# Kernel optimization log

Hardware: AMD Instinct MI355X
Metric: run time of the kernel (lower is better)

Reference implementation:

```python
import jax, jax.numpy as jnp
import numpy as np

N_HEADS, N_LEVELS, N_POINTS, D_MODEL = 8, 4, 4, 256
HEAD_DIM = D_MODEL // N_HEADS
SPATIAL = np.array([[128, 128], [64, 64], [32, 32], [16, 16]], dtype=np.int32)
LEN_IN = int((SPATIAL[:, 0] * SPATIAL[:, 1]).sum())  # 21760
B = 2


def setup_inputs() -> dict:
    key = jax.random.key(0)
    ks = jax.random.split(key, 8)
    level_start = np.concatenate([[0], np.cumsum(SPATIAL[:, 0] * SPATIAL[:, 1])[:-1]]).astype(np.int32)
    return {
        "query": jax.random.normal(ks[0], (B, LEN_IN, D_MODEL), jnp.float32),
        "reference_points": jax.random.uniform(ks[1], (B, LEN_IN, 2), jnp.float32),
        "input_flatten": jax.random.normal(ks[2], (B, LEN_IN, D_MODEL), jnp.float32),
        "spatial_shapes": jnp.asarray(SPATIAL),
        "level_start_index": jnp.asarray(level_start),
        "W_off": jax.random.normal(ks[3], (D_MODEL, N_HEADS * N_LEVELS * N_POINTS * 2), jnp.float32) * 0.02,
        "b_off": jnp.zeros((N_HEADS * N_LEVELS * N_POINTS * 2,), jnp.float32),
        "W_attn": jax.random.normal(ks[4], (D_MODEL, N_HEADS * N_LEVELS * N_POINTS), jnp.float32) * 0.02,
        "b_attn": jnp.zeros((N_HEADS * N_LEVELS * N_POINTS,), jnp.float32),
        "W_out": jax.random.normal(ks[5], (D_MODEL, D_MODEL), jnp.float32) * 0.02,
        "b_out": jnp.zeros((D_MODEL,), jnp.float32),
    }


def _ms_deform_attn(query, reference_points, input_flatten, spatial_np,
                    W_off, b_off, W_attn, b_attn, W_out, b_out):
    Bq, Lq, C = query.shape
    # sampling offsets / attention weights projections (GEMMs)
    off = (query @ W_off + b_off).reshape(Bq, Lq, N_HEADS, N_LEVELS, N_POINTS, 2)
    attn = (query @ W_attn + b_attn).reshape(Bq, Lq, N_HEADS, N_LEVELS * N_POINTS)
    attn = jax.nn.softmax(attn, axis=-1).reshape(Bq, Lq, N_HEADS, N_LEVELS, N_POINTS)
    # offset normalizer is (W, H) per level
    norm = jnp.asarray(spatial_np[:, ::-1].copy(), jnp.float32)  # [L,2]
    # normalized sampling locations (x,y) in [0,1]: [B,Lq,h,L,p,2]
    loc = reference_points[:, :, None, None, None, :] + off / norm[None, None, None, :, None, :]

    b_idx = jnp.arange(Bq)[:, None, None, None]
    h_idx = jnp.arange(N_HEADS)[None, None, :, None]
    out = jnp.zeros((Bq, Lq, N_HEADS, HEAD_DIM), query.dtype)
    start = 0
    for lvl in range(N_LEVELS):
        H, W = int(spatial_np[lvl, 0]), int(spatial_np[lvl, 1])
        feat = input_flatten[:, start:start + H * W].reshape(Bq, H, W, N_HEADS, HEAD_DIM)
        start += H * W
        # grid_sample(align_corners=False): pixel = loc * size - 0.5
        x = loc[:, :, :, lvl, :, 0] * W - 0.5  # [B,Lq,h,p]
        y = loc[:, :, :, lvl, :, 1] * H - 0.5
        x0 = jnp.floor(x); y0 = jnp.floor(y)
        fx = x - x0; fy = y - y0
        x0i = x0.astype(jnp.int32); y0i = y0.astype(jnp.int32)

        def gather(ix, iy):
            valid = (ix >= 0) & (ix < W) & (iy >= 0) & (iy < H)  # zero padding
            ixc = jnp.clip(ix, 0, W - 1); iyc = jnp.clip(iy, 0, H - 1)
            v = feat[b_idx, iyc, ixc, h_idx]  # [B,Lq,h,p,hd]
            return v * valid[..., None].astype(v.dtype)

        v00 = gather(x0i, y0i)
        v01 = gather(x0i + 1, y0i)
        v10 = gather(x0i, y0i + 1)
        v11 = gather(x0i + 1, y0i + 1)
        sampled = (v00 * ((1 - fx) * (1 - fy))[..., None]
                   + v01 * (fx * (1 - fy))[..., None]
                   + v10 * ((1 - fx) * fy)[..., None]
                   + v11 * (fx * fy)[..., None])  # [B,Lq,h,p,hd]
        out = out + (sampled * attn[:, :, :, lvl, :, None]).sum(axis=3)
    return out.reshape(Bq, Lq, C) @ W_out + b_out


def reference(query, reference_points, input_flatten, spatial_shapes, level_start_index,
              W_off, b_off, W_attn, b_attn, W_out, b_out):
    spatial_np = np.asarray(jax.device_get(spatial_shapes))
    return _ms_deform_attn(query, reference_points, input_flatten, spatial_np,
                           W_off, b_off, W_attn, b_attn, W_out, b_out)
```

## Files before the change

### kernel.cpp

```cpp
#include <hip/hip_runtime.h>
#include <hip/hip_fp16.h>
#include <math.h>

#define BATCH   2
#define LQ      21760
#define CDIM    256
#define NHEADS  8
#define NLEV    4
#define NPTS    4
#define HDIM    32
#define NPROJ   384
#define QT      16
#define PROJ_LD 388
#define NTUP    (QT * NHEADS * NLEV * NPTS)

typedef short  bf16x8 __attribute__((ext_vector_type(8)));
typedef float  f32x4  __attribute__((ext_vector_type(4)));

static __device__ __host__ inline unsigned short f2bf(float x) {
    unsigned int u = __builtin_bit_cast(unsigned int, x);
    unsigned int r = (u + 0x7fff + ((u >> 16) & 1)) >> 16;
    return (unsigned short)r;
}
static __device__ inline unsigned int pack2h(float a, float b) {
    __half2 h = __floats2half2_rn(a, b);
    return __builtin_bit_cast(unsigned int, h);
}
static __device__ inline float2 unpack2h(unsigned int u) {
    return __half22float2(__builtin_bit_cast(__half2, u));
}

__global__ __launch_bounds__(256) void pack_w(
    const float* __restrict__ Woff, const float* __restrict__ Wattn,
    const float* __restrict__ Wout, unsigned short* __restrict__ ws)
{
    const int id = blockIdx.x * 256 + threadIdx.x;
    bf16x8 pk;
    if (id < 12288) {
        const int lane = id & 63, s = (id >> 6) & 7, tn = id >> 9;
        const int col = tn * 16 + (lane & 15);
        const int k0  = s * 32 + (lane >> 4) * 8;
        #pragma unroll
        for (int i = 0; i < 8; ++i) {
            const int k = k0 + i;
            const float w = (col < 256) ? Woff[(size_t)k * 256 + col]
                                        : Wattn[(size_t)k * 128 + (col - 256)];
            pk[i] = (short)f2bf(w);
        }
        *(bf16x8*)(ws + (size_t)id * 8) = pk;
    } else {
        const int id2 = id - 12288;
        const int lane = id2 & 63, s = (id2 >> 6) & 7, tn = id2 >> 9;
        const int col = tn * 16 + (lane & 15);
        const int k0  = s * 32 + (lane >> 4) * 8;
        #pragma unroll
        for (int i = 0; i < 8; ++i)
            pk[i] = (short)f2bf(Wout[(size_t)(k0 + i) * 256 + col]);
        *(bf16x8*)(ws + (size_t)(12288 + id2) * 8) = pk;
    }
}

static __device__ inline void load_afrags(const unsigned char* xqb, int lane, bf16x8* af) {
    const int row = lane & 15;
    const int kg8 = (lane >> 4) * 8;
    const int sw  = (row & 7) << 4;
    const int base = row * 512;
    #pragma unroll
    for (int s = 0; s < 8; ++s) {
        const int byte = base + (((s * 32 + kg8) * 2) ^ sw);
        af[s] = *(const bf16x8*)(xqb + byte);
    }
}

__global__ __launch_bounds__(256, 4) void msda_fused(
    const float* __restrict__ query,
    const float* __restrict__ refp,
    const float* __restrict__ feat,
    const float* __restrict__ boff,
    const float* __restrict__ battn,
    const float* __restrict__ bout,
    const unsigned short* __restrict__ wsB,
    const unsigned short* __restrict__ wsO,
    float* __restrict__ out)
{
    __shared__ __align__(16) unsigned char xqb[QT * 512];
    __shared__ __align__(16) float proj[QT * PROJ_LD];
    __shared__ float rp[QT][2];

    const int t    = threadIdx.x;
    const int lane = t & 63;
    const int wid  = t >> 6;
    const int q0   = blockIdx.x * QT;
    const int b    = q0 / LQ;

    #define PROJ(q, c) proj[(q) * PROJ_LD + (c)]
    int*          toff = (int*)proj;
    unsigned int* tw01 = (unsigned int*)proj + NTUP;
    unsigned int* tw23 = (unsigned int*)proj + 2 * NTUP;

    {
        const float4* src = (const float4*)(query + (size_t)q0 * CDIM);
        #pragma unroll
        for (int i = 0; i < 4; ++i) {
            const int idx = t + i * 256;
            const int row = idx >> 6;
            const int k4  = (idx & 63) * 4;
            const float4 v = src[idx];
            uint2 w;
            w.x = (unsigned int)f2bf(v.x) | ((unsigned int)f2bf(v.y) << 16);
            w.y = (unsigned int)f2bf(v.z) | ((unsigned int)f2bf(v.w) << 16);
            const int byte = row * 512 + (((k4 * 2)) ^ ((row & 7) << 4));
            *(uint2*)(xqb + byte) = w;
        }
        if (t < QT * 2) ((float*)rp)[t] = refp[(size_t)q0 * 2 + t];
    }
    __syncthreads();

    {
        bf16x8 af[8];
        load_afrags(xqb, lane, af);
        const int colb = lane & 15;
        const int r0   = (lane >> 4) * 4;
        #pragma unroll
        for (int j = 0; j < 6; ++j) {
            const int tn  = wid * 6 + j;
            const int col = tn * 16 + colb;
            const float bv = (col < 256) ? boff[col] : battn[col - 256];
            f32x4 acc = {bv, bv, bv, bv};
            const bf16x8* bp = (const bf16x8*)wsB + (size_t)tn * 8 * 64 + lane;
            #pragma unroll
            for (int s = 0; s < 8; ++s)
                acc = __builtin_amdgcn_mfma_f32_16x16x32_bf16(af[s], bp[(size_t)s * 64], acc, 0, 0, 0);
            #pragma unroll
            for (int r = 0; r < 4; ++r) PROJ(r0 + r, col) = acc[r];
        }
    }
    __syncthreads();

    if (t < QT * NHEADS) {
        const int q = t >> 3, h = t & 7;
        float* a = &PROJ(q, CDIM + h * 16);
        float m = a[0];
        #pragma unroll
        for (int j = 1; j < 16; ++j) m = fmaxf(m, a[j]);
        float e[16], s = 0.f;
        #pragma unroll
        for (int j = 0; j < 16; ++j) { e[j] = __expf(a[j] - m); s += e[j]; }
        const float inv = 1.f / s;
        #pragma unroll
        for (int j = 0; j < 16; ++j) a[j] = e[j] * inv;
    }
    __syncthreads();

    int   r_off[8];
    unsigned int r_w01[8], r_w23[8];
    {
        const int LW[4] = {128, 64, 32, 16};
        const int LS[4] = {0, 16384, 20480, 21504};
        #pragma unroll
        for (int k = 0; k < 8; ++k) {
            const int tupid = t * 8 + k;
            const int q  = tupid >> 7;
            const int h  = (tupid >> 4) & 7;
            const int lp = tupid & 15;
            const int l  = lp >> 2, p = lp & 3;
            const int Wl = LW[l], Hl = LW[l];
            const float ox = PROJ(q, ((h * NLEV + l) * NPTS + p) * 2 + 0);
            const float oy = PROJ(q, ((h * NLEV + l) * NPTS + p) * 2 + 1);
            const float aw = PROJ(q, CDIM + h * 16 + lp);
            const float x = rp[q][0] * (float)Wl + ox - 0.5f;
            const float y = rp[q][1] * (float)Hl + oy - 0.5f;
            const float x0f = floorf(x), y0f = floorf(y);
            const float fx = x - x0f, fy = y - y0f;
            const int ix = (int)x0f, iy = (int)y0f;
            const bool vx0 = (ix >= 0) & (ix < Wl), vx1 = (ix >= -1) & (ix < Wl - 1);
            const bool vy0 = (iy >= 0) & (iy < Hl), vy1 = (iy >= -1) & (iy < Hl - 1);
            const float w00 = (vx0 & vy0) ? (1.f - fx) * (1.f - fy) * aw : 0.f;
            const float w01 = (vx1 & vy0) ? fx * (1.f - fy) * aw : 0.f;
            const float w10 = (vx0 & vy1) ? (1.f - fx) * fy * aw : 0.f;
            const float w11 = (vx1 & vy1) ? fx * fy * aw : 0.f;
            r_off[k] = LS[l] + iy * Wl + ix;
            r_w01[k] = pack2h(w00, w01);
            r_w23[k] = pack2h(w10, w11);
        }
    }
    __syncthreads();
    #pragma unroll
    for (int k = 0; k < 8; ++k) {
        const int tupid = t * 8 + k;
        toff[tupid] = r_off[k];
        tw01[tupid] = r_w01[k];
        tw23[tupid] = r_w23[k];
    }
    __syncthreads();

    {
        const int qg = t >> 6, h = (t >> 3) & 7, d4 = t & 7;
        const float* featb = feat + (size_t)b * LQ * CDIM + h * HDIM + d4 * 4;
        #pragma unroll
        for (int j = 0; j < 4; ++j) {
            const int q = qg * 4 + j;
            const int tbase = (q * 8 + h) * 16;
            f32x4 acc = {0.f, 0.f, 0.f, 0.f};
            #pragma unroll
            for (int lp = 0; lp < 16; ++lp) {
                const int Wl = (lp < 4) ? 128 : (lp < 8) ? 64 : (lp < 12) ? 32 : 16;
                const int off00 = toff[tbase + lp];
                const float2 wlo = unpack2h(tw01[tbase + lp]);
                const float2 whi = unpack2h(tw23[tbase + lp]);
                const int o0 = (wlo.x != 0.f) ? off00          : 0;
                const int o1 = (wlo.y != 0.f) ? off00 + 1      : 0;
                const int o2 = (whi.x != 0.f) ? off00 + Wl     : 0;
                const int o3 = (whi.y != 0.f) ? off00 + Wl + 1 : 0;
                const f32x4 v0 = *(const f32x4*)(featb + (long)o0 * CDIM);
                const f32x4 v1 = *(const f32x4*)(featb + (long)o1 * CDIM);
                const f32x4 v2 = *(const f32x4*)(featb + (long)o2 * CDIM);
                const f32x4 v3 = *(const f32x4*)(featb + (long)o3 * CDIM);
                acc += wlo.x * v0;
                acc += wlo.y * v1;
                acc += whi.x * v2;
                acc += whi.y * v3;
            }
            uint2 wv;
            wv.x = (unsigned int)f2bf(acc[0]) | ((unsigned int)f2bf(acc[1]) << 16);
            wv.y = (unsigned int)f2bf(acc[2]) | ((unsigned int)f2bf(acc[3]) << 16);
            const int byte = q * 512 + (((h * HDIM + d4 * 4) * 2) ^ ((q & 7) << 4));
            *(uint2*)(xqb + byte) = wv;
        }
    }
    __syncthreads();

    {
        bf16x8 af[8];
        load_afrags(xqb, lane, af);
        const int colb = lane & 15;
        const int r0   = (lane >> 4) * 4;
        #pragma unroll
        for (int j = 0; j < 4; ++j) {
            const int tn  = wid * 4 + j;
            const int col = tn * 16 + colb;
            const float bv = bout[col];
            f32x4 acc = {bv, bv, bv, bv};
            const bf16x8* bp = (const bf16x8*)wsO + (size_t)tn * 8 * 64 + lane;
            #pragma unroll
            for (int s = 0; s < 8; ++s)
                acc = __builtin_amdgcn_mfma_f32_16x16x32_bf16(af[s], bp[(size_t)s * 64], acc, 0, 0, 0);
            #pragma unroll
            for (int r = 0; r < 4; ++r)
                out[(size_t)(q0 + r0 + r) * CDIM + col] = acc[r];
        }
    }
    #undef PROJ
}

extern "C" void kernel_launch(void* const* d_in, const int* in_sizes, int n_in,
                              void* d_out, int out_size, void* d_ws, size_t ws_size,
                              hipStream_t stream) {
    const float* query = (const float*)d_in[0];
    const float* refp  = (const float*)d_in[1];
    const float* feat  = (const float*)d_in[2];
    const float* Woff  = (const float*)d_in[5];
    const float* boff  = (const float*)d_in[6];
    const float* Wattn = (const float*)d_in[7];
    const float* battn = (const float*)d_in[8];
    const float* Wout  = (const float*)d_in[9];
    const float* bout  = (const float*)d_in[10];
    float* out = (float*)d_out;

    unsigned short* ws = (unsigned short*)d_ws;
    const unsigned short* wsB = ws;
    const unsigned short* wsO = ws + (size_t)12288 * 8;

    hipLaunchKernelGGL(pack_w, dim3(80), dim3(256), 0, stream, Woff, Wattn, Wout, ws);

    const int nrows = BATCH * LQ;
    hipLaunchKernelGGL(msda_fused, dim3(nrows / QT), dim3(256), 0, stream,
                       query, refp, feat, boff, battn, bout, wsB, wsO, out);
}
```

Baseline: 159.1 us.

## Pre-pack features to bf16, shuffle sampling tuples via registers, fp16 projection LDS

Adds a pre-pass that converts the value tensor to bf16 in workspace, so the bilinear gather reads half the bytes per sample. Sampling offsets and weights are passed between lanes with wave shuffles instead of being staged in shared memory. The projection buffer is stored as fp16, which shrinks LDS use enough to raise the occupancy hint to 5 blocks per CU. In exchange, every call pays a full extra read and write of the feature tensor, and offsets and weights lose precision; an fp32 fallback path remains for when the workspace is too small.

```diff
diff --git a/kernel.cpp b/kernel.cpp
--- a/kernel.cpp
+++ b/kernel.cpp
@@ -9,13 +9,13 @@
 #define NLEV    4
 #define NPTS    4
 #define HDIM    32
-#define NPROJ   384
 #define QT      16
-#define PROJ_LD 388
-#define NTUP    (QT * NHEADS * NLEV * NPTS)
+#define PROJ_LDH 392
 
 typedef short  bf16x8 __attribute__((ext_vector_type(8)));
 typedef float  f32x4  __attribute__((ext_vector_type(4)));
+typedef unsigned int u32x4 __attribute__((ext_vector_type(4)));
+typedef unsigned short u16x8 __attribute__((ext_vector_type(8)));
 
 static __device__ __host__ inline unsigned short f2bf(float x) {
     unsigned int u = __builtin_bit_cast(unsigned int, x);
@@ -29,10 +29,29 @@
 static __device__ inline float2 unpack2h(unsigned int u) {
     return __half22float2(__builtin_bit_cast(__half2, u));
 }
+static __device__ inline float bfhi(unsigned int u) {
+    return __builtin_bit_cast(float, u & 0xffff0000u);
+}
+static __device__ inline float bflo(unsigned int u) {
+    return __builtin_bit_cast(float, u << 16);
+}
+
+__global__ __launch_bounds__(256) void pack_feat(
+    const float* __restrict__ f, unsigned short* __restrict__ o)
+{
+    const size_t i8 = ((size_t)blockIdx.x * 256 + threadIdx.x) * 8;
+    const float4 v0 = *(const float4*)(f + i8);
+    const float4 v1 = *(const float4*)(f + i8 + 4);
+    u16x8 pk;
+    pk[0] = f2bf(v0.x); pk[1] = f2bf(v0.y); pk[2] = f2bf(v0.z); pk[3] = f2bf(v0.w);
+    pk[4] = f2bf(v1.x); pk[5] = f2bf(v1.y); pk[6] = f2bf(v1.z); pk[7] = f2bf(v1.w);
+    *(u16x8*)(o + i8) = pk;
+}
 
 __global__ __launch_bounds__(256) void pack_w(
     const float* __restrict__ Woff, const float* __restrict__ Wattn,
-    const float* __restrict__ Wout, unsigned short* __restrict__ ws)
+    const float* __restrict__ Wout, unsigned short* __restrict__ wsB,
+    unsigned short* __restrict__ wsO)
 {
     const int id = blockIdx.x * 256 + threadIdx.x;
     bf16x8 pk;
@@ -47,7 +66,7 @@
                                         : Wattn[(size_t)k * 128 + (col - 256)];
             pk[i] = (short)f2bf(w);
         }
-        *(bf16x8*)(ws + (size_t)id * 8) = pk;
+        *(bf16x8*)(wsB + (size_t)id * 8) = pk;
     } else {
         const int id2 = id - 12288;
         const int lane = id2 & 63, s = (id2 >> 6) & 7, tn = id2 >> 9;
@@ -56,7 +75,7 @@
         #pragma unroll
         for (int i = 0; i < 8; ++i)
             pk[i] = (short)f2bf(Wout[(size_t)(k0 + i) * 256 + col]);
-        *(bf16x8*)(ws + (size_t)(12288 + id2) * 8) = pk;
+        *(bf16x8*)(wsO + (size_t)id2 * 8) = pk;
     }
 }
 
@@ -72,10 +91,12 @@
     }
 }
 
-__global__ __launch_bounds__(256, 4) void msda_fused(
+template<bool BF16F>
+__global__ __launch_bounds__(256, 5) void msda_fused(
     const float* __restrict__ query,
     const float* __restrict__ refp,
     const float* __restrict__ feat,
+    const unsigned short* __restrict__ featbf,
     const float* __restrict__ boff,
     const float* __restrict__ battn,
     const float* __restrict__ bout,
@@ -84,19 +105,13 @@
     float* __restrict__ out)
 {
     __shared__ __align__(16) unsigned char xqb[QT * 512];
-    __shared__ __align__(16) float proj[QT * PROJ_LD];
-    __shared__ float rp[QT][2];
+    __shared__ __align__(16) __half projh[QT * PROJ_LDH];
 
     const int t    = threadIdx.x;
     const int lane = t & 63;
     const int wid  = t >> 6;
     const int q0   = blockIdx.x * QT;
     const int b    = q0 / LQ;
-
-    #define PROJ(q, c) proj[(q) * PROJ_LD + (c)]
-    int*          toff = (int*)proj;
-    unsigned int* tw01 = (unsigned int*)proj + NTUP;
-    unsigned int* tw23 = (unsigned int*)proj + 2 * NTUP;
 
     {
         const float4* src = (const float4*)(query + (size_t)q0 * CDIM);
@@ -109,10 +124,9 @@
             uint2 w;
             w.x = (unsigned int)f2bf(v.x) | ((unsigned int)f2bf(v.y) << 16);
             w.y = (unsigned int)f2bf(v.z) | ((unsigned int)f2bf(v.w) << 16);
-            const int byte = row * 512 + (((k4 * 2)) ^ ((row & 7) << 4));
+            const int byte = row * 512 + ((k4 * 2) ^ ((row & 7) << 4));
             *(uint2*)(xqb + byte) = w;
         }
-        if (t < QT * 2) ((float*)rp)[t] = refp[(size_t)q0 * 2 + t];
     }
     __syncthreads();
 
@@ -132,44 +146,50 @@
             for (int s = 0; s < 8; ++s)
                 acc = __builtin_amdgcn_mfma_f32_16x16x32_bf16(af[s], bp[(size_t)s * 64], acc, 0, 0, 0);
             #pragma unroll
-            for (int r = 0; r < 4; ++r) PROJ(r0 + r, col) = acc[r];
+            for (int r = 0; r < 4; ++r)
+                projh[(r0 + r) * PROJ_LDH + col] = __float2half(acc[r]);
         }
     }
     __syncthreads();
 
     if (t < QT * NHEADS) {
         const int q = t >> 3, h = t & 7;
-        float* a = &PROJ(q, CDIM + h * 16);
-        float m = a[0];
-        #pragma unroll
-        for (int j = 1; j < 16; ++j) m = fmaxf(m, a[j]);
-        float e[16], s = 0.f;
-        #pragma unroll
-        for (int j = 0; j < 16; ++j) { e[j] = __expf(a[j] - m); s += e[j]; }
+        __half* a = projh + q * PROJ_LDH + 256 + h * 16;
+        float v[16];
+        #pragma unroll
+        for (int j = 0; j < 16; ++j) v[j] = __half2float(a[j]);
+        float m = v[0];
+        #pragma unroll
+        for (int j = 1; j < 16; ++j) m = fmaxf(m, v[j]);
+        float s = 0.f;
+        #pragma unroll
+        for (int j = 0; j < 16; ++j) { v[j] = __expf(v[j] - m); s += v[j]; }
         const float inv = 1.f / s;
         #pragma unroll
-        for (int j = 0; j < 16; ++j) a[j] = e[j] * inv;
+        for (int j = 0; j < 16; ++j) a[j] = __float2half(v[j] * inv);
     }
     __syncthreads();
 
-    int   r_off[8];
-    unsigned int r_w01[8], r_w23[8];
-    {
+    int r_off[8]; int r_w01[8]; int r_w23[8];
+    {
+        const int q_own = t >> 4;
+        const int h_own = (t >> 1) & 7;
+        const int lpb   = (t & 1) * 8;
+        const float rx = refp[(size_t)(q0 + q_own) * 2 + 0];
+        const float ry = refp[(size_t)(q0 + q_own) * 2 + 1];
         const int LW[4] = {128, 64, 32, 16};
         const int LS[4] = {0, 16384, 20480, 21504};
         #pragma unroll
         for (int k = 0; k < 8; ++k) {
-            const int tupid = t * 8 + k;
-            const int q  = tupid >> 7;
-            const int h  = (tupid >> 4) & 7;
-            const int lp = tupid & 15;
-            const int l  = lp >> 2, p = lp & 3;
+            const int lp = lpb + k;
+            const int l = lp >> 2, p = lp & 3;
             const int Wl = LW[l], Hl = LW[l];
-            const float ox = PROJ(q, ((h * NLEV + l) * NPTS + p) * 2 + 0);
-            const float oy = PROJ(q, ((h * NLEV + l) * NPTS + p) * 2 + 1);
-            const float aw = PROJ(q, CDIM + h * 16 + lp);
-            const float x = rp[q][0] * (float)Wl + ox - 0.5f;
-            const float y = rp[q][1] * (float)Hl + oy - 0.5f;
+            const unsigned int oxy = *(const unsigned int*)(projh + q_own * PROJ_LDH
+                                        + ((h_own * NLEV + l) * NPTS + p) * 2);
+            const float2 oo = unpack2h(oxy);
+            const float aw = __half2float(projh[q_own * PROJ_LDH + 256 + h_own * 16 + lp]);
+            const float x = rx * (float)Wl + oo.x - 0.5f;
+            const float y = ry * (float)Hl + oo.y - 0.5f;
             const float x0f = floorf(x), y0f = floorf(y);
             const float fx = x - x0f, fy = y - y0f;
             const int ix = (int)x0f, iy = (int)y0f;
@@ -180,52 +200,92 @@
             const float w10 = (vx0 & vy1) ? (1.f - fx) * fy * aw : 0.f;
             const float w11 = (vx1 & vy1) ? fx * fy * aw : 0.f;
             r_off[k] = LS[l] + iy * Wl + ix;
-            r_w01[k] = pack2h(w00, w01);
-            r_w23[k] = pack2h(w10, w11);
-        }
-    }
-    __syncthreads();
-    #pragma unroll
-    for (int k = 0; k < 8; ++k) {
-        const int tupid = t * 8 + k;
-        toff[tupid] = r_off[k];
-        tw01[tupid] = r_w01[k];
-        tw23[tupid] = r_w23[k];
-    }
-    __syncthreads();
-
-    {
-        const int qg = t >> 6, h = (t >> 3) & 7, d4 = t & 7;
-        const float* featb = feat + (size_t)b * LQ * CDIM + h * HDIM + d4 * 4;
-        #pragma unroll
-        for (int j = 0; j < 4; ++j) {
-            const int q = qg * 4 + j;
-            const int tbase = (q * 8 + h) * 16;
-            f32x4 acc = {0.f, 0.f, 0.f, 0.f};
+            r_w01[k] = (int)pack2h(w00, w01);
+            r_w23[k] = (int)pack2h(w10, w11);
+        }
+    }
+
+    {
+        const int d8   = t & 3;
+        const int h    = (t >> 2) & 7;
+        const int qpar = (t >> 5) & 1;
+        const int qg   = t >> 6;
+        const int chb  = h * HDIM + d8 * 8;
+        #pragma unroll
+        for (int j = 0; j < 2; ++j) {
+            const int q = qg * 4 + j * 2 + qpar;
+            const int srcb = (q & 3) * 16 + h * 2;
+            float a0 = 0.f, a1 = 0.f, a2 = 0.f, a3 = 0.f;
+            float a4 = 0.f, a5 = 0.f, a6 = 0.f, a7 = 0.f;
             #pragma unroll
             for (int lp = 0; lp < 16; ++lp) {
+                const int k = lp & 7;
+                const int src = srcb + (lp >> 3);
                 const int Wl = (lp < 4) ? 128 : (lp < 8) ? 64 : (lp < 12) ? 32 : 16;
-                const int off00 = toff[tbase + lp];
-                const float2 wlo = unpack2h(tw01[tbase + lp]);
-                const float2 whi = unpack2h(tw23[tbase + lp]);
+                const int off00 = __shfl(r_off[k], src);
+                const float2 wlo = unpack2h((unsigned int)__shfl(r_w01[k], src));
+                const float2 whi = unpack2h((unsigned int)__shfl(r_w23[k], src));
                 const int o0 = (wlo.x != 0.f) ? off00          : 0;
                 const int o1 = (wlo.y != 0.f) ? off00 + 1      : 0;
                 const int o2 = (whi.x != 0.f) ? off00 + Wl     : 0;
                 const int o3 = (whi.y != 0.f) ? off00 + Wl + 1 : 0;
-                const f32x4 v0 = *(const f32x4*)(featb + (long)o0 * CDIM);
-                const f32x4 v1 = *(const f32x4*)(featb + (long)o1 * CDIM);
-                const f32x4 v2 = *(const f32x4*)(featb + (long)o2 * CDIM);
-                const f32x4 v3 = *(const f32x4*)(featb + (long)o3 * CDIM);
-                acc += wlo.x * v0;
-                acc += wlo.y * v1;
-                acc += whi.x * v2;
-                acc += whi.y * v3;
+                if (BF16F) {
+                    const unsigned short* fb = featbf + (size_t)b * LQ * CDIM + chb;
+                    const u32x4 v0 = *(const u32x4*)(fb + (long)o0 * CDIM);
+                    const u32x4 v1 = *(const u32x4*)(fb + (long)o1 * CDIM);
+                    const u32x4 v2 = *(const u32x4*)(fb + (long)o2 * CDIM);
+                    const u32x4 v3 = *(const u32x4*)(fb + (long)o3 * CDIM);
+                    a0 = fmaf(wlo.x, bflo(v0[0]), a0); a1 = fmaf(wlo.x, bfhi(v0[0]), a1);
+                    a2 = fmaf(wlo.x, bflo(v0[1]), a2); a3 = fmaf(wlo.x, bfhi(v0[1]), a3);
+                    a4 = fmaf(wlo.x, bflo(v0[2]), a4); a5 = fmaf(wlo.x, bfhi(v0[2]), a5);
+                    a6 = fmaf(wlo.x, bflo(v0[3]), a6); a7 = fmaf(wlo.x, bfhi(v0[3]), a7);
+                    a0 = fmaf(wlo.y, bflo(v1[0]), a0); a1 = fmaf(wlo.y, bfhi(v1[0]), a1);
+                    a2 = fmaf(wlo.y, bflo(v1[1]), a2); a3 = fmaf(wlo.y, bfhi(v1[1]), a3);
+                    a4 = fmaf(wlo.y, bflo(v1[2]), a4); a5 = fmaf(wlo.y, bfhi(v1[2]), a5);
+                    a6 = fmaf(wlo.y, bflo(v1[3]), a6); a7 = fmaf(wlo.y, bfhi(v1[3]), a7);
+                    a0 = fmaf(whi.x, bflo(v2[0]), a0); a1 = fmaf(whi.x, bfhi(v2[0]), a1);
+                    a2 = fmaf(whi.x, bflo(v2[1]), a2); a3 = fmaf(whi.x, bfhi(v2[1]), a3);
+                    a4 = fmaf(whi.x, bflo(v2[2]), a4); a5 = fmaf(whi.x, bfhi(v2[2]), a5);
+                    a6 = fmaf(whi.x, bflo(v2[3]), a6); a7 = fmaf(whi.x, bfhi(v2[3]), a7);
+                    a0 = fmaf(whi.y, bflo(v3[0]), a0); a1 = fmaf(whi.y, bfhi(v3[0]), a1);
+                    a2 = fmaf(whi.y, bflo(v3[1]), a2); a3 = fmaf(whi.y, bfhi(v3[1]), a3);
+                    a4 = fmaf(whi.y, bflo(v3[2]), a4); a5 = fmaf(whi.y, bfhi(v3[2]), a5);
+                    a6 = fmaf(whi.y, bflo(v3[3]), a6); a7 = fmaf(whi.y, bfhi(v3[3]), a7);
+                } else {
+                    const float* fb = feat + (size_t)b * LQ * CDIM + chb;
+                    const f32x4 v0a = *(const f32x4*)(fb + (long)o0 * CDIM);
+                    const f32x4 v0b = *(const f32x4*)(fb + (long)o0 * CDIM + 4);
+                    const f32x4 v1a = *(const f32x4*)(fb + (long)o1 * CDIM);
+                    const f32x4 v1b = *(const f32x4*)(fb + (long)o1 * CDIM + 4);
+                    const f32x4 v2a = *(const f32x4*)(fb + (long)o2 * CDIM);
+                    const f32x4 v2b = *(const f32x4*)(fb + (long)o2 * CDIM + 4);
+                    const f32x4 v3a = *(const f32x4*)(fb + (long)o3 * CDIM);
+                    const f32x4 v3b = *(const f32x4*)(fb + (long)o3 * CDIM + 4);
+                    a0 = fmaf(wlo.x, v0a[0], a0); a1 = fmaf(wlo.x, v0a[1], a1);
+                    a2 = fmaf(wlo.x, v0a[2], a2); a3 = fmaf(wlo.x, v0a[3], a3);
+                    a4 = fmaf(wlo.x, v0b[0], a4); a5 = fmaf(wlo.x, v0b[1], a5);
+                    a6 = fmaf(wlo.x, v0b[2], a6); a7 = fmaf(wlo.x, v0b[3], a7);
+                    a0 = fmaf(wlo.y, v1a[0], a0); a1 = fmaf(wlo.y, v1a[1], a1);
+                    a2 = fmaf(wlo.y, v1a[2], a2); a3 = fmaf(wlo.y, v1a[3], a3);
+                    a4 = fmaf(wlo.y, v1b[0], a4); a5 = fmaf(wlo.y, v1b[1], a5);
+                    a6 = fmaf(wlo.y, v1b[2], a6); a7 = fmaf(wlo.y, v1b[3], a7);
+                    a0 = fmaf(whi.x, v2a[0], a0); a1 = fmaf(whi.x, v2a[1], a1);
+                    a2 = fmaf(whi.x, v2a[2], a2); a3 = fmaf(whi.x, v2a[3], a3);
+                    a4 = fmaf(whi.x, v2b[0], a4); a5 = fmaf(whi.x, v2b[1], a5);
+                    a6 = fmaf(whi.x, v2b[2], a6); a7 = fmaf(whi.x, v2b[3], a7);
+                    a0 = fmaf(whi.y, v3a[0], a0); a1 = fmaf(whi.y, v3a[1], a1);
+                    a2 = fmaf(whi.y, v3a[2], a2); a3 = fmaf(whi.y, v3a[3], a3);
+                    a4 = fmaf(whi.y, v3b[0], a4); a5 = fmaf(whi.y, v3b[1], a5);
+                    a6 = fmaf(whi.y, v3b[2], a6); a7 = fmaf(whi.y, v3b[3], a7);
+                }
             }
-            uint2 wv;
-            wv.x = (unsigned int)f2bf(acc[0]) | ((unsigned int)f2bf(acc[1]) << 16);
-            wv.y = (unsigned int)f2bf(acc[2]) | ((unsigned int)f2bf(acc[3]) << 16);
-            const int byte = q * 512 + (((h * HDIM + d4 * 4) * 2) ^ ((q & 7) << 4));
-            *(uint2*)(xqb + byte) = wv;
+            u32x4 wv;
+            wv[0] = (unsigned int)f2bf(a0) | ((unsigned int)f2bf(a1) << 16);
+            wv[1] = (unsigned int)f2bf(a2) | ((unsigned int)f2bf(a3) << 16);
+            wv[2] = (unsigned int)f2bf(a4) | ((unsigned int)f2bf(a5) << 16);
+            wv[3] = (unsigned int)f2bf(a6) | ((unsigned int)f2bf(a7) << 16);
+            const int byte = q * 512 + (((chb) * 2) ^ ((q & 7) << 4));
+            *(u32x4*)(xqb + byte) = wv;
         }
     }
     __syncthreads();
@@ -250,7 +310,6 @@
                 out[(size_t)(q0 + r0 + r) * CDIM + col] = acc[r];
         }
     }
-    #undef PROJ
 }
 
 extern "C" void kernel_launch(void* const* d_in, const int* in_sizes, int n_in,
@@ -268,12 +327,25 @@
     float* out = (float*)d_out;
 
     unsigned short* ws = (unsigned short*)d_ws;
-    const unsigned short* wsB = ws;
-    const unsigned short* wsO = ws + (size_t)12288 * 8;
-
-    hipLaunchKernelGGL(pack_w, dim3(80), dim3(256), 0, stream, Woff, Wattn, Wout, ws);
+    const size_t feat_us = (size_t)BATCH * LQ * CDIM;
+    const size_t need    = (feat_us + 98304 + 65536) * 2;
+    const bool usebf = ws_size >= need;
 
     const int nrows = BATCH * LQ;
-    hipLaunchKernelGGL(msda_fused, dim3(nrows / QT), dim3(256), 0, stream,
-                       query, refp, feat, boff, battn, bout, wsB, wsO, out);
-}
+
+    if (usebf) {
+        unsigned short* featbf = ws;
+        unsigned short* wsB = ws + feat_us;
+        unsigned short* wsO = wsB + 98304;
+        pack_feat<<<dim3((unsigned)(feat_us / 8 / 256)), dim3(256), 0, stream>>>(feat, featbf);
+        pack_w<<<dim3(80), dim3(256), 0, stream>>>(Woff, Wattn, Wout, wsB, wsO);
+        msda_fused<true><<<dim3(nrows / QT), dim3(256), 0, stream>>>(
+            query, refp, feat, featbf, boff, battn, bout, wsB, wsO, out);
+    } else {
+        unsigned short* wsB = ws;
+        unsigned short* wsO = ws + 98304;
+        pack_w<<<dim3(80), dim3(256), 0, stream>>>(Woff, Wattn, Wout, wsB, wsO);
+        msda_fused<false><<<dim3(nrows / QT), dim3(256), 0, stream>>>(
+            query, refp, feat, (const unsigned short*)nullptr, boff, battn, bout, wsB, wsO, out);
+    }
+}
```

Measured after the change: 144.4 us. 9.2% less time.
